# Performance work log

Hardware: AMD Instinct MI355X
Metric: run time of the kernel (lower is better)

The kernel has to match this reference:

```python
import jax, jax.numpy as jnp
import numpy as np

N, A, AD, D, H, KTOP = 5, 900, 8, 256, 8, 300


def _bbox_min_max(anchor):
    # anchor: [N,A,8] = x,y,z,logw,logl,logh,sin_yaw,cos_yaw
    xyz = anchor[..., :3]
    w, l, h = [jnp.exp(anchor[..., i]) for i in (3, 4, 5)]
    sy, cy = anchor[..., 6], anchor[..., 7]
    yaw = jnp.arctan2(sy, cy)
    ca, sa = jnp.abs(jnp.cos(yaw)), jnp.abs(jnp.sin(yaw))
    ex = 0.5 * (l * ca + w * sa)
    ey = 0.5 * (l * sa + w * ca)
    half = jnp.stack([ex, ey, 0.5 * h], axis=-1)
    return xyz - half, xyz + half


def _forward(i2j_anchor, b_anchor, b_feature, transform_matrix, anchor_embed,
             w_roi, b_roi, bn_g, bn_b, fc1_w, fc1_b, fc2_w, fc2_b,
             anc_w, anc_b, lam_w, lam_b, wq, bq, wk, bk, wv, bv, wo, bo,
             ln_g, ln_b, K):
    n, a, ad = b_anchor.shape
    d = b_feature.shape[-1]
    heads = lam_w.shape[-1]
    dh = d // heads
    # ROI scoring + topk selection of anchors to broadcast to neighbors
    roi = jax.nn.sigmoid(b_feature @ w_roi + b_roi)[..., 0]              # [N,A]
    top_scores, top_idx = jax.lax.top_k(roi, K)                          # [N,K]
    conf = top_scores > 0.5                                              # [N,K]
    nbr = jnp.take_along_axis(b_feature, top_idx[..., None], axis=1)     # [N,K,D]
    idx4 = jnp.broadcast_to(top_idx[None, :, :, None], (n, n, K, ad))
    i2j_sel = jnp.take_along_axis(i2j_anchor, idx4, axis=2)              # [N,N,K,AD]
    # remove self (eye-mask): off-diagonal j per row i, row-major order
    offdiag = np.array([[j for j in range(n) if j != i] for i in range(n)])
    rows = np.arange(n)[:, None]
    m = K * (n - 1)
    i2j_rm = i2j_sel[rows, offdiag].reshape(n, m, ad)                    # [N,M,AD]
    tm_rm = transform_matrix[rows, offdiag]                              # [N,N-1,4,4]
    key_feat = nbr[offdiag].reshape(n, m, d)                             # [N,M,D]
    conf_rm = conf[offdiag].reshape(n, m, 1)
    nf_masked = key_feat * conf_rm
    # bbox-range masked aggregation of neighbor features into ego anchors
    mn, mx = _bbox_min_max(b_anchor)                                     # [N,A,3]
    centers = i2j_rm[..., :3]                                            # [N,M,3]
    inside = jnp.all((centers[:, None, :, :] >= mn[:, :, None, :]) &
                     (centers[:, None, :, :] <= mx[:, :, None, :]), axis=-1)  # [N,A,M]
    agg = jnp.einsum('nam,nmd->nad', inside.astype(b_feature.dtype), nf_masked)
    is_greater_than_range = ~jnp.any(inside, axis=1)                     # [N,M]
    b_feature = b_feature + agg
    # transform-matrix encoding: first 3 rows of 4x4 -> BN -> MLP
    mlp_in = tm_rm[:, :, :3, :].reshape(-1, 12)
    mu = mlp_in.mean(0)
    var = mlp_in.var(0)
    xbn = (mlp_in - mu) / jnp.sqrt(var + 1e-5) * bn_g + bn_b
    t = jax.nn.relu(xbn @ fc1_w + fc1_b) @ fc2_w + fc2_b                 # [N*(N-1),D]
    trans_enc = jnp.repeat(t.reshape(n, n - 1, 1, d), K, axis=2).reshape(n, m, d)
    key_pos = i2j_rm @ anc_w + anc_b + trans_enc                         # anchorencoder + trans
    # distance-biased attention mask
    diff = b_anchor[:, :, None, :2] - i2j_rm[:, None, :, :2]
    dist = jnp.sqrt(jnp.sum(diff * diff, axis=-1) + 1e-12)               # cdist [N,A,M]
    lm = (b_feature @ lam_w + lam_b).transpose(0, 2, 1)                  # [N,H,A]
    bias = -jnp.log1p(dist)[:, None, :, :] * lm[..., None]               # [N,H,A,M]
    # multi-head attention (query=b_feature(+anchor_embed pos), key/value=neighbors)
    q = b_feature + anchor_embed
    k = key_feat + key_pos
    v = key_feat
    qh = (q @ wq + bq).reshape(n, a, heads, dh)
    kh = (k @ wk + bk).reshape(n, m, heads, dh)
    vh = (v @ wv + bv).reshape(n, m, heads, dh)
    logits = jnp.einsum('nahd,nmhd->nham', qh, kh) / np.sqrt(dh).astype(np.float32) + bias
    attn = jax.nn.softmax(logits, axis=-1)
    out = jnp.einsum('nham,nmhd->nahd', attn, vh).reshape(n, a, d) @ wo + bo
    res = b_feature + out                                                # residual (identity=query)
    mu2 = res.mean(-1, keepdims=True)
    var2 = res.var(-1, keepdims=True)
    return (res - mu2) / jnp.sqrt(var2 + 1e-5) * ln_g + ln_b


def setup_inputs() -> dict:
    key = jax.random.key(0)
    ks = jax.random.split(key, 24)
    s = 0.05
    inp = {
        'i2j_anchor': jax.random.normal(ks[0], (N, N, A, AD), jnp.float32),
        'b_anchor': jax.random.normal(ks[1], (N, A, AD), jnp.float32),
        'b_feature': jax.random.normal(ks[2], (N, A, D), jnp.float32),
        'transform_matrix': jax.random.normal(ks[3], (N, N, 4, 4), jnp.float32),
        'anchor_embed': jax.random.normal(ks[4], (N, A, D), jnp.float32),
        'w_roi': jax.random.normal(ks[5], (D, 1), jnp.float32) * s,
        'b_roi': jnp.zeros((1,), jnp.float32),
        'bn_g': jnp.ones((12,), jnp.float32),
        'bn_b': jnp.zeros((12,), jnp.float32),
        'fc1_w': jax.random.normal(ks[6], (12, D), jnp.float32) * s,
        'fc1_b': jnp.zeros((D,), jnp.float32),
        'fc2_w': jax.random.normal(ks[7], (D, D), jnp.float32) * s,
        'fc2_b': jnp.zeros((D,), jnp.float32),
        'anc_w': jax.random.normal(ks[8], (AD, D), jnp.float32) * s,
        'anc_b': jnp.zeros((D,), jnp.float32),
        'lam_w': jax.random.normal(ks[9], (D, H), jnp.float32) * s,
        'lam_b': jnp.zeros((H,), jnp.float32),
        'wq': jax.random.normal(ks[10], (D, D), jnp.float32) * s,
        'bq': jnp.zeros((D,), jnp.float32),
        'wk': jax.random.normal(ks[11], (D, D), jnp.float32) * s,
        'bk': jnp.zeros((D,), jnp.float32),
        'wv': jax.random.normal(ks[12], (D, D), jnp.float32) * s,
        'bv': jnp.zeros((D,), jnp.float32),
        'wo': jax.random.normal(ks[13], (D, D), jnp.float32) * s,
        'bo': jnp.zeros((D,), jnp.float32),
        'ln_g': jnp.ones((D,), jnp.float32),
        'ln_b': jnp.zeros((D,), jnp.float32),
        'K': KTOP,
    }
    return inp


def reference(i2j_anchor, b_anchor, b_feature, transform_matrix, anchor_embed,
              w_roi, b_roi, bn_g, bn_b, fc1_w, fc1_b, fc2_w, fc2_b,
              anc_w, anc_b, lam_w, lam_b, wq, bq, wk, bk, wv, bv, wo, bo,
              ln_g, ln_b, K):
    return _forward(i2j_anchor, b_anchor, b_feature, transform_matrix, anchor_embed,
                    w_roi, b_roi, bn_g, bn_b, fc1_w, fc1_b, fc2_w, fc2_b,
                    anc_w, anc_b, lam_w, lam_b, wq, bq, wk, bk, wv, bv, wo, bo,
                    ln_g, ln_b, K)
```

## Files before the change

### kernel.cpp

```cpp
#include <hip/hip_runtime.h>
#include <math.h>

#define N_ 5
#define A_ 900
#define AD_ 8
#define D_ 256
#define H_ 8
#define DH_ 32
#define K_ 300
#define NM1_ 4
#define M_ 1200
#define MP_ 1216
#define KC_ 64
#define HALF_ 600
#define NCHUNK2_ 10

typedef _Float16 f16x8 __attribute__((ext_vector_type(8)));
typedef _Float16 f16x4 __attribute__((ext_vector_type(4)));
typedef float f32x4 __attribute__((ext_vector_type(4)));

__global__ __launch_bounds__(256) void score_kernel(const float* __restrict__ bf,
                                                    const float* __restrict__ w,
                                                    const float* __restrict__ b,
                                                    float* __restrict__ scores) {
  int wid = threadIdx.x >> 6, lane = threadIdx.x & 63;
  int row = blockIdx.x * 4 + wid;
  if (row >= N_ * A_) return;
  const float* x = bf + (long)row * D_;
  float dot = 0.f;
#pragma unroll
  for (int t = 0; t < 4; t++) dot += x[lane + 64 * t] * w[lane + 64 * t];
#pragma unroll
  for (int o = 32; o; o >>= 1) dot += __shfl_xor(dot, o, 64);
  if (lane == 0) scores[row] = 1.0f / (1.0f + expf(-(dot + b[0])));
}

__global__ __launch_bounds__(1024) void topk_kernel(const float* __restrict__ scores,
                                                    int* __restrict__ top_idx,
                                                    float* __restrict__ conf) {
  __shared__ float sc[1024];
  __shared__ int si[1024];
  int i = blockIdx.x, t = threadIdx.x;
  sc[t] = (t < A_) ? scores[i * A_ + t] : -INFINITY;
  si[t] = t;
  __syncthreads();
  for (int k = 2; k <= 1024; k <<= 1) {
    for (int j = k >> 1; j > 0; j >>= 1) {
      int ixj = t ^ j;
      if (ixj > t) {
        bool dir = ((t & k) == 0);
        float a = sc[t], b = sc[ixj];
        bool sw = dir ? (a < b) : (a > b);
        if (sw) {
          sc[t] = b; sc[ixj] = a;
          int tmp = si[t]; si[t] = si[ixj]; si[ixj] = tmp;
        }
      }
      __syncthreads();
    }
  }
  if (t < K_) {
    top_idx[i * K_ + t] = si[t];
    conf[i * K_ + t] = sc[t] > 0.5f ? 1.0f : 0.0f;
  }
}

__global__ __launch_bounds__(256) void mlp_kernel(const float* __restrict__ tm,
                                                  const float* __restrict__ bn_g, const float* __restrict__ bn_b,
                                                  const float* __restrict__ fc1_w, const float* __restrict__ fc1_b,
                                                  const float* __restrict__ fc2_w, const float* __restrict__ fc2_b,
                                                  float* __restrict__ t_out) {
  int r = blockIdx.x;
  int t = threadIdx.x;
  __shared__ float x[20][12];
  __shared__ float y[12];
  __shared__ float hbuf[D_];
  if (t < 240) {
    int rr = t / 12, f = t % 12;
    int i = rr / NM1_, jj = rr % NM1_;
    int j = jj < i ? jj : jj + 1;
    int r4 = f / 4, c4 = f % 4;
    x[rr][f] = tm[((long)(i * N_ + j) * 4 + r4) * 4 + c4];
  }
  __syncthreads();
  if (t < 12) {
    float s = 0.f;
    for (int rr = 0; rr < 20; rr++) s += x[rr][t];
    float m = s / 20.0f;
    float v = 0.f;
    for (int rr = 0; rr < 20; rr++) { float d = x[rr][t] - m; v += d * d; }
    v /= 20.0f;
    y[t] = (x[r][t] - m) * rsqrtf(v + 1e-5f) * bn_g[t] + bn_b[t];
  }
  __syncthreads();
  float acc = fc1_b[t];
#pragma unroll
  for (int f = 0; f < 12; f++) acc += y[f] * fc1_w[f * D_ + t];
  hbuf[t] = fmaxf(acc, 0.0f);
  __syncthreads();
  float acc2 = fc2_b[t];
  for (int k = 0; k < D_; k++) acc2 += hbuf[k] * fc2_w[k * D_ + t];
  t_out[r * D_ + t] = acc2;
}

#define GKT_ 30
__global__ __launch_bounds__(256) void gather_kernel(const float* __restrict__ b_feature,
                                                     const float* __restrict__ i2j_anchor,
                                                     const int* __restrict__ top_idx,
                                                     const float* __restrict__ conf,
                                                     const float* __restrict__ anc_w,
                                                     const float* __restrict__ anc_b,
                                                     const float* __restrict__ t_mlp,
                                                     _Float16* __restrict__ key_feat16,
                                                     float* __restrict__ conf_rm,
                                                     float* __restrict__ i2j_rm,
                                                     _Float16* __restrict__ key_in16) {
  int blk = blockIdx.x;
  int i = blk / NM1_, jj = blk % NM1_;
  int j = jj < i ? jj : jj + 1;
  int k0 = blockIdx.y * GKT_;
  int c = threadIdx.x;
  __shared__ float aw[AD_][D_];
#pragma unroll
  for (int r = 0; r < AD_; r++) aw[r][c] = anc_w[r * D_ + c];
  float ab = anc_b[c];
  float tv = t_mlp[(i * NM1_ + jj) * D_ + c];
  __syncthreads();
  for (int k = k0; k < k0 + GKT_; k++) {
    int idx = top_idx[j * K_ + k];
    float cf = conf[j * K_ + k];
    const float* src = b_feature + ((long)(j * A_ + idx)) * D_;
    float val = src[c];
    long mrow = (long)i * M_ + jj * K_ + k;
    key_feat16[mrow * D_ + c] = (_Float16)val;
    const float* ap = i2j_anchor + ((long)((i * N_ + j) * A_ + idx)) * AD_;
    if (c < AD_) i2j_rm[mrow * AD_ + c] = ap[c];
    if (c == 0) conf_rm[mrow] = cf;
    float pos = ab + tv;
#pragma unroll
    for (int r = 0; r < AD_; r++) pos += ap[r] * aw[r][c];
    key_in16[mrow * D_ + c] = (_Float16)(val + pos);
  }
}

__global__ __launch_bounds__(256) void trans_kernel(const float* __restrict__ w0, const float* __restrict__ w1,
                                                    const float* __restrict__ w2, const float* __restrict__ w3,
                                                    const _Float16* __restrict__ kf,
                                                    _Float16* __restrict__ wT, _Float16* __restrict__ kT) {
  int bid = blockIdx.x;
  int t = threadIdx.x;
  if (bid < 64) {
    int y = bid >> 4, tile = bid & 15;
    const float* src = (y == 0) ? w0 : (y == 1) ? w1 : (y == 2) ? w2 : w3;
    _Float16* dst = wT + (size_t)y * D_ * D_;
    int kr = (tile >> 2) * 64, nc = (tile & 3) * 64;
    __shared__ float lds[64][65];
#pragma unroll
    for (int r = 0; r < 16; r++) {
      int row = r * 4 + (t >> 6), col = t & 63;
      lds[row][col] = src[(size_t)(kr + row) * D_ + nc + col];
    }
    __syncthreads();
#pragma unroll
    for (int r = 0; r < 16; r++) {
      int orow = r * 4 + (t >> 6), ocol = t & 63;
      dst[(size_t)(nc + orow) * D_ + kr + ocol] = (_Float16)lds[ocol][orow];
    }
  } else {
    int b = bid - 64;
    int i = b / 76, rem = b % 76;
    int m0 = (rem % 19) * 64, d0 = (rem / 19) * 64;
    __shared__ _Float16 lds2[64][66];
    const _Float16* src = kf + (size_t)i * M_ * D_;
    _Float16* dst = kT + (size_t)i * D_ * M_;
#pragma unroll
    for (int r = 0; r < 16; r++) {
      int row = r * 4 + (t >> 6), col = t & 63;
      int m = m0 + row;
      lds2[row][col] = (m < M_) ? src[(size_t)m * D_ + d0 + col] : (_Float16)0.0f;
    }
    __syncthreads();
#pragma unroll
    for (int r = 0; r < 16; r++) {
      int orow = r * 4 + (t >> 6), ocol = t & 63;
      int m = m0 + ocol;
      if (m < M_) dst[(size_t)(d0 + orow) * M_ + m] = lds2[ocol][orow];
    }
  }
}

__global__ __launch_bounds__(256) void insbias_kernel(const float* __restrict__ i2j_rm,
                                                      const float* __restrict__ conf_rm,
                                                      const float* __restrict__ ban,
                                                      _Float16* __restrict__ inside,
                                                      _Float16* __restrict__ Lbuf) {
  int i = blockIdx.x;
  int g = blockIdx.y;
  __shared__ float cx[M_], cy[M_], cz[M_], cf[M_];
  for (int m = threadIdx.x; m < M_; m += 256) {
    const float* cp = i2j_rm + ((long)i * M_ + m) * AD_;
    cx[m] = cp[0]; cy[m] = cp[1]; cz[m] = cp[2];
    cf[m] = conf_rm[(long)i * M_ + m];
  }
  __syncthreads();
#pragma unroll
  for (int r = 0; r < 4; r++) {
    int a = g * 4 + r;
    int row = i * A_ + a;
    const float* ap = ban + (long)row * AD_;
    float ax = ap[0], ay = ap[1], az = ap[2];
    float w = expf(ap[3]), l = expf(ap[4]), hh = expf(ap[5]);
    float yaw = atan2f(ap[6], ap[7]);
    float ca = fabsf(cosf(yaw)), sa = fabsf(sinf(yaw));
    float ex = 0.5f * (l * ca + w * sa);
    float ey = 0.5f * (l * sa + w * ca);
    float ez = 0.5f * hh;
    float mn0 = ax - ex, mn1 = ay - ey, mn2 = az - ez;
    float mx0 = ax + ex, mx1 = ay + ey, mx2 = az + ez;
    _Float16* ldst = Lbuf + (size_t)row * MP_;
    _Float16* idst = inside + (size_t)row * M_;
    for (int m = threadIdx.x; m < M_; m += 256) {
      float c0 = cx[m], c1 = cy[m], c2 = cz[m];
      bool ins = (c0 >= mn0) && (c0 <= mx0) && (c1 >= mn1) && (c1 <= mx1) && (c2 >= mn2) && (c2 <= mx2);
      idst[m] = ins ? (_Float16)cf[m] : (_Float16)0.0f;
      float dx = ax - c0, dy = ay - c1;
      ldst[m] = (_Float16)log1pf(sqrtf(dx * dx + dy * dy + 1e-12f));
    }
  }
}

#define GLD_ 74
template <typename TO, bool HAS_BIAS, bool HAS_RES>
__device__ __forceinline__ void gemm_tile_body(
    const _Float16* __restrict__ A, int lda, int Mr,
    const _Float16* __restrict__ B, int ldb,
    const float* __restrict__ bias, const float* __restrict__ res,
    TO* __restrict__ C, int ldc,
    int m0, int n0, int k_begin, int k_end) {
  __shared__ _Float16 As[64 * GLD_];
  __shared__ _Float16 Bs[64 * GLD_];
  int tid = threadIdx.x;
  int lane = tid & 63;
  int wid = tid >> 6;
  int wr = (wid >> 1) * 32, wc = (wid & 1) * 32;
  int lr = lane & 15, lk = (lane >> 4) * 8;
  int srow = tid >> 3;
  int scol = (tid & 7) * 8;
  f16x8 aR[2], bR[2];
  f16x8 zero8 = {};
  auto loadg = [&](int kb) {
#pragma unroll
    for (int r = 0; r < 2; r++) {
      int gm = m0 + srow + r * 32;
      int gk = kb + scol;
      aR[r] = (gm < Mr && gk < k_end) ? *(const f16x8*)&A[(size_t)gm * lda + gk] : zero8;
      int gn = n0 + srow + r * 32;
      bR[r] = (gk < k_end) ? *(const f16x8*)&B[(size_t)gn * ldb + gk] : zero8;
    }
  };
  auto store_lds = [&]() {
#pragma unroll
    for (int r = 0; r < 2; r++) {
      *(f16x8*)&As[(srow + r * 32) * GLD_ + scol] = aR[r];
      *(f16x8*)&Bs[(srow + r * 32) * GLD_ + scol] = bR[r];
    }
  };
  f32x4 acc[2][2] = {};
  int niter = (k_end - k_begin + 63) >> 6;
  loadg(k_begin);
  store_lds();
  __syncthreads();
  for (int it = 0; it < niter; ++it) {
    bool more = (it + 1 < niter);
    if (more) loadg(k_begin + (it + 1) * 64);
#pragma unroll
    for (int ks = 0; ks < 2; ks++) {
      f16x8 af[2], bf[2];
#pragma unroll
      for (int mi = 0; mi < 2; mi++) af[mi] = *(const f16x8*)&As[(wr + mi * 16 + lr) * GLD_ + ks * 32 + lk];
#pragma unroll
      for (int ni = 0; ni < 2; ni++) bf[ni] = *(const f16x8*)&Bs[(wc + ni * 16 + lr) * GLD_ + ks * 32 + lk];
#pragma unroll
      for (int mi = 0; mi < 2; mi++)
#pragma unroll
        for (int ni = 0; ni < 2; ni++)
          acc[mi][ni] = __builtin_amdgcn_mfma_f32_16x16x32_f16(af[mi], bf[ni], acc[mi][ni], 0, 0, 0);
    }
    __syncthreads();
    if (more) { store_lds(); __syncthreads(); }
  }
#pragma unroll
  for (int mi = 0; mi < 2; mi++)
#pragma unroll
    for (int ni = 0; ni < 2; ni++)
#pragma unroll
      for (int rr = 0; rr < 4; rr++) {
        int row = m0 + wr + mi * 16 + (lane >> 4) * 4 + rr;
        int col = n0 + wc + ni * 16 + lr;
        if (row < Mr) {
          float v = acc[mi][ni][rr];
          if (HAS_BIAS) v += bias[col];
          if (HAS_RES) v += res[(size_t)row * ldc + col];
          C[(size_t)row * ldc + col] = (TO)v;
        }
      }
}

__global__ __launch_bounds__(256) void agg_kernel(const _Float16* __restrict__ inside16,
                                                  const _Float16* __restrict__ kT16,
                                                  float* __restrict__ partial) {
  int i = blockIdx.z >> 2, sk = blockIdx.z & 3;
  int kb = sk * 320;
  int ke = kb + 320 < M_ ? kb + 320 : M_;
  gemm_tile_body<float, false, false>(
      inside16 + (size_t)i * A_ * M_, M_, A_,
      kT16 + (size_t)i * D_ * M_, M_,
      nullptr, nullptr,
      partial + (size_t)(sk * N_ + i) * A_ * D_, D_,
      blockIdx.x * 64, blockIdx.y * 64, kb, ke);
}

__global__ __launch_bounds__(256) void agg_reduce(const float* __restrict__ partial,
                                                  const float* __restrict__ b_feature,
                                                  const float* __restrict__ anchor_embed,
                                                  const float* __restrict__ lam_w,
                                                  const float* __restrict__ lam_b,
                                                  float* __restrict__ bf_upd,
                                                  _Float16* __restrict__ qin16,
                                                  float* __restrict__ lm_rm) {
  int wid = threadIdx.x >> 6, lane = threadIdx.x & 63;
  int rg = blockIdx.x * 4 + wid;
  int d0 = lane * 4;
  float lw[4][8];
#pragma unroll
  for (int e = 0; e < 4; e++) {
#pragma unroll
    for (int h = 0; h < 8; h++) lw[e][h] = lam_w[(d0 + e) * 8 + h];
  }
  float4 s = *(const float4*)&partial[(size_t)rg * D_ + d0];
#pragma unroll
  for (int sk = 1; sk < 4; sk++) {
    float4 p = *(const float4*)&partial[((size_t)sk * N_ * A_ + rg) * D_ + d0];
    s.x += p.x; s.y += p.y; s.z += p.z; s.w += p.w;
  }
  float4 bf = *(const float4*)&b_feature[(size_t)rg * D_ + d0];
  s.x += bf.x; s.y += bf.y; s.z += bf.z; s.w += bf.w;
  *(float4*)&bf_upd[(size_t)rg * D_ + d0] = s;
  float4 ae = *(const float4*)&anchor_embed[(size_t)rg * D_ + d0];
  f16x4 q4;
  q4[0] = (_Float16)(s.x + ae.x); q4[1] = (_Float16)(s.y + ae.y);
  q4[2] = (_Float16)(s.z + ae.z); q4[3] = (_Float16)(s.w + ae.w);
  *(f16x4*)&qin16[(size_t)rg * D_ + d0] = q4;
  float sv[4] = {s.x, s.y, s.z, s.w};
  float acc[8] = {};
#pragma unroll
  for (int e = 0; e < 4; e++)
#pragma unroll
    for (int h = 0; h < 8; h++) acc[h] += sv[e] * lw[e][h];
#pragma unroll
  for (int h = 0; h < 8; h++) {
#pragma unroll
    for (int o = 32; o; o >>= 1) acc[h] += __shfl_xor(acc[h], o, 64);
  }
  if (lane == 0) {
#pragma unroll
    for (int h = 0; h < 8; h++) lm_rm[(size_t)rg * H_ + h] = acc[h] + lam_b[h];
  }
}

__global__ __launch_bounds__(256) void qkv_kernel(const _Float16* __restrict__ qA,
                                                  const _Float16* __restrict__ kA,
                                                  const _Float16* __restrict__ vA,
                                                  const _Float16* __restrict__ wT,
                                                  const float* __restrict__ bq,
                                                  const float* __restrict__ bk,
                                                  const float* __restrict__ bv,
                                                  _Float16* __restrict__ qC,
                                                  _Float16* __restrict__ kC,
                                                  _Float16* __restrict__ vC) {
  int bid = blockIdx.x;
  const _Float16 *Ap, *Bp;
  const float* bias;
  _Float16* Cp;
  int Mr, t, mt, nt;
  if (bid < 284)      { Ap = qA; Bp = wT;               bias = bq; Cp = qC; Mr = 4500; t = bid;       mt = t % 71; nt = t / 71; }
  else if (bid < 660) { Ap = kA; Bp = wT + D_ * D_;     bias = bk; Cp = kC; Mr = 6000; t = bid - 284; mt = t % 94; nt = t / 94; }
  else                { Ap = vA; Bp = wT + 2 * D_ * D_; bias = bv; Cp = vC; Mr = 6000; t = bid - 660; mt = t % 94; nt = t / 94; }
  gemm_tile_body<_Float16, true, false>(Ap, D_, Mr, Bp, D_, bias, nullptr, Cp, D_, mt * 64, nt * 64, 0, D_);
}

__global__ __launch_bounds__(256) void outp_kernel(const _Float16* __restrict__ att16,
                                                   const _Float16* __restrict__ woT,
                                                   float* __restrict__ partial2) {
  int bid = blockIdx.x;
  int sk = bid >= 284 ? 1 : 0;
  int t = bid - sk * 284;
  int mt = t % 71, nt = t / 71;
  gemm_tile_body<float, false, false>(att16, D_, 4500, woT, D_, nullptr, nullptr,
                                      partial2 + (size_t)sk * 4500 * D_, D_,
                                      mt * 64, nt * 64, sk * 128, sk * 128 + 128);
}

__global__ __launch_bounds__(256) void attn_mfma(const _Float16* __restrict__ qh16,
                                                 const _Float16* __restrict__ kh16,
                                                 const _Float16* __restrict__ vh16,
                                                 const float* __restrict__ lm_rm,
                                                 const _Float16* __restrict__ Lbuf,
                                                 float* __restrict__ part_ms,
                                                 float* __restrict__ part_o) {
  int bid = blockIdx.x;
  int wgid = (bid & 7) * 150 + (bid >> 3);
  int ih = wgid / 30;
  int rest = wgid % 30;
  int half = rest / 15, qt = rest % 15;
  int i = ih >> 3, h = ih & 7;
  int a0 = qt * 64;
  int mbase = half * HALF_;
  int mlimit = mbase + HALF_;

  __shared__ _Float16 QP[64][74];
  __shared__ _Float16 Ks[64][42];
  __shared__ _Float16 Vt[32][74];
  __shared__ _Float16 Ls[64][74];
  __shared__ float lmvs[64];

  int tid = threadIdx.x;
  int lane = tid & 63;
  int w16 = (tid >> 6) * 16;
  int lr = lane & 15;
  int lk = (lane >> 4) * 8;
  int srow = tid >> 2, spiece = tid & 3;
  int lrow = tid >> 3, lpc = (tid & 7) * 8;

  {
    int aq = a0 + srow;
    int a_ld = aq < A_ ? aq : A_ - 1;
    const uint4* src = (const uint4*)(qh16 + ((long)(i * A_ + a_ld) * D_ + h * DH_));
    *(uint4*)&QP[srow][spiece * 8] = src[spiece];
  }
  if (tid < 64) {
    int aq = a0 + tid;
    int a_ld = aq < A_ ? aq : A_ - 1;
    lmvs[tid] = lm_rm[(long)(i * A_ + a_ld) * H_ + h];
  }

  const _Float16* kb = kh16 + (long)i * M_ * D_ + h * DH_;
  const _Float16* vb = vh16 + (long)i * M_ * D_ + h * DH_;
  const _Float16* lptr[2];
#pragma unroll
  for (int rr = 0; rr < 2; rr++) {
    int aq = a0 + lrow + rr * 32;
    int a_ld = aq < A_ ? aq : A_ - 1;
    lptr[rr] = Lbuf + (size_t)(i * A_ + a_ld) * MP_ + lpc;
  }

  uint4 kvR, vvR;
  f16x8 lR[2];
  auto loadr = [&](int c) {
    int m0 = mbase + c * KC_;
    int mrow = m0 + srow;
    if (mrow < M_) {
      kvR = ((const uint4*)(kb + (long)mrow * D_))[spiece];
      vvR = ((const uint4*)(vb + (long)mrow * D_))[spiece];
    } else {
      kvR = make_uint4(0, 0, 0, 0);
      vvR = make_uint4(0, 0, 0, 0);
    }
#pragma unroll
    for (int rr = 0; rr < 2; rr++) lR[rr] = *(const f16x8*)&lptr[rr][m0];
  };

  __syncthreads();

  float lmr[4];
#pragma unroll
  for (int r = 0; r < 4; r++) lmr[r] = lmvs[w16 + (lane >> 4) * 4 + r];
  f16x8 qa = *(const f16x8*)&QP[w16 + lr][lk];

  float m_run[4], s_part[4];
  f32x4 oacc[2] = {};
#pragma unroll
  for (int r = 0; r < 4; r++) { m_run[r] = -INFINITY; s_part[r] = 0.0f; }

  loadr(0);

  for (int c = 0; c < NCHUNK2_; c++) {
    int m0 = mbase + c * KC_;
    __syncthreads();
    *(uint4*)&Ks[srow][spiece * 8] = kvR;
    {
      const _Float16* hp = (const _Float16*)&vvR;
#pragma unroll
      for (int e = 0; e < 8; e++) Vt[spiece * 8 + e][srow] = hp[e];
    }
#pragma unroll
    for (int rr = 0; rr < 2; rr++) *(f16x8*)&Ls[lrow + rr * 32][lpc] = lR[rr];
    if (c + 1 < NCHUNK2_) loadr(c + 1);
    __syncthreads();

    f32x4 sacc[4];
#pragma unroll
    for (int mb = 0; mb < 4; mb++) {
      f16x8 kf = *(const f16x8*)&Ks[mb * 16 + lr][lk];
      sacc[mb] = __builtin_amdgcn_mfma_f32_16x16x32_f16(qa, kf, (f32x4){0.f, 0.f, 0.f, 0.f}, 0, 0, 0);
    }

    float lg[4][4];
#pragma unroll
    for (int mb = 0; mb < 4; mb++) {
      int mcol = m0 + mb * 16 + (lane & 15);
      bool valid = (mcol < mlimit);
#pragma unroll
      for (int r = 0; r < 4; r++) {
        int qrow = w16 + (lane >> 4) * 4 + r;
        float L = (float)Ls[qrow][mb * 16 + (lane & 15)];
        float v = sacc[mb][r] * 0.17677669529663687f - L * lmr[r];
        lg[mb][r] = valid ? v : -INFINITY;
      }
    }
#pragma unroll
    for (int r = 0; r < 4; r++) {
      float cm = fmaxf(fmaxf(lg[0][r], lg[1][r]), fmaxf(lg[2][r], lg[3][r]));
#pragma unroll
      for (int o = 1; o < 16; o <<= 1) cm = fmaxf(cm, __shfl_xor(cm, o, 64));
      float nm = fmaxf(m_run[r], cm);
      float corr = __expf(m_run[r] - nm);
      s_part[r] *= corr;
      oacc[0][r] *= corr;
      oacc[1][r] *= corr;
      m_run[r] = nm;
      float ps = 0.0f;
#pragma unroll
      for (int mb = 0; mb < 4; mb++) {
        float p = __expf(lg[mb][r] - nm);
        ps += p;
        QP[w16 + (lane >> 4) * 4 + r][mb * 16 + (lane & 15)] = (_Float16)p;
      }
      s_part[r] += ps;
    }

#pragma unroll
    for (int ks = 0; ks < 2; ks++) {
      f16x8 pa = *(const f16x8*)&QP[w16 + lr][ks * 32 + lk];
#pragma unroll
      for (int db = 0; db < 2; db++) {
        f16x8 vf = *(const f16x8*)&Vt[db * 16 + lr][ks * 32 + lk];
        oacc[db] = __builtin_amdgcn_mfma_f32_16x16x32_f16(pa, vf, oacc[db], 0, 0, 0);
      }
    }
  }

  size_t base = (size_t)(half * 40 + ih) * A_;
#pragma unroll
  for (int r = 0; r < 4; r++) {
    float st = s_part[r];
#pragma unroll
    for (int o = 1; o < 16; o <<= 1) st += __shfl_xor(st, o, 64);
    int a = a0 + w16 + (lane >> 4) * 4 + r;
    if (a < A_) {
      size_t rowb = base + a;
      if ((lane & 15) == 0) {
        part_ms[rowb * 2 + 0] = m_run[r];
        part_ms[rowb * 2 + 1] = st;
      }
      part_o[rowb * 32 + (lane & 15)] = oacc[0][r];
      part_o[rowb * 32 + 16 + (lane & 15)] = oacc[1][r];
    }
  }
}

__global__ __launch_bounds__(256) void attn_merge(const float* __restrict__ part_ms,
                                                  const float* __restrict__ part_o,
                                                  _Float16* __restrict__ att16) {
  int t = threadIdx.x;
  int R = blockIdx.x * 8 + (t >> 5);
  int d = t & 31;
  int ih = R / A_, a = R % A_;
  int i = ih >> 3, h = ih & 7;
  size_t r0 = (size_t)ih * A_ + a;
  size_t r1 = (size_t)(40 + ih) * A_ + a;
  float m0 = part_ms[r0 * 2], s0 = part_ms[r0 * 2 + 1];
  float m1 = part_ms[r1 * 2], s1 = part_ms[r1 * 2 + 1];
  float M = fmaxf(m0, m1);
  float e0 = __expf(m0 - M), e1 = __expf(m1 - M);
  float inv = 1.0f / (s0 * e0 + s1 * e1);
  float o = part_o[r0 * 32 + d] * e0 + part_o[r1 * 32 + d] * e1;
  att16[((size_t)(i * A_ + a)) * D_ + h * DH_ + d] = (_Float16)(o * inv);
}

__global__ __launch_bounds__(256) void ln_kernel(const float* __restrict__ partial2,
                                                 const float* __restrict__ bo,
                                                 const float* __restrict__ resid,
                                                 const float* __restrict__ g,
                                                 const float* __restrict__ b,
                                                 float* __restrict__ out) {
  int row = blockIdx.x;
  int t = threadIdx.x;
  size_t idx = (size_t)row * D_ + t;
  float v = partial2[idx] + partial2[(size_t)4500 * D_ + idx] + bo[t] + resid[idx];
  float s = v, sq = v * v;
#pragma unroll
  for (int o = 32; o; o >>= 1) {
    s += __shfl_xor(s, o, 64);
    sq += __shfl_xor(sq, o, 64);
  }
  __shared__ float ss[4], ssq[4];
  int wid = t >> 6, lane = t & 63;
  if (lane == 0) { ss[wid] = s; ssq[wid] = sq; }
  __syncthreads();
  float ts = ss[0] + ss[1] + ss[2] + ss[3];
  float tq = ssq[0] + ssq[1] + ssq[2] + ssq[3];
  float mean = ts / (float)D_;
  float var = tq / (float)D_ - mean * mean;
  out[idx] = (v - mean) * rsqrtf(var + 1e-5f) * g[t] + b[t];
}

extern "C" void kernel_launch(void* const* d_in, const int* in_sizes, int n_in,
                              void* d_out, int out_size, void* d_ws, size_t ws_size,
                              hipStream_t stream) {
  const float* i2j_anchor   = (const float*)d_in[0];
  const float* b_anchor     = (const float*)d_in[1];
  const float* b_feature    = (const float*)d_in[2];
  const float* tm           = (const float*)d_in[3];
  const float* anchor_embed = (const float*)d_in[4];
  const float* w_roi  = (const float*)d_in[5];
  const float* b_roi  = (const float*)d_in[6];
  const float* bn_g   = (const float*)d_in[7];
  const float* bn_b   = (const float*)d_in[8];
  const float* fc1_w  = (const float*)d_in[9];
  const float* fc1_b  = (const float*)d_in[10];
  const float* fc2_w  = (const float*)d_in[11];
  const float* fc2_b  = (const float*)d_in[12];
  const float* anc_w  = (const float*)d_in[13];
  const float* anc_b  = (const float*)d_in[14];
  const float* lam_w  = (const float*)d_in[15];
  const float* lam_b  = (const float*)d_in[16];
  const float* wq = (const float*)d_in[17];
  const float* bq = (const float*)d_in[18];
  const float* wk = (const float*)d_in[19];
  const float* bk = (const float*)d_in[20];
  const float* wv = (const float*)d_in[21];
  const float* bv = (const float*)d_in[22];
  const float* wo = (const float*)d_in[23];
  const float* bo = (const float*)d_in[24];
  const float* ln_g = (const float*)d_in[25];
  const float* ln_b = (const float*)d_in[26];

  float* ws = (float*)d_ws;
  size_t off = 0;
  auto alloc = [&](size_t n) { float* p = ws + off; off += (n + 3) & ~(size_t)3; return p; };

  float* scores     = alloc(N_ * A_);
  int*   top_idx    = (int*)alloc(N_ * K_);
  float* conf       = alloc(N_ * K_);
  float* t_mlp      = alloc(20 * D_);
  float* conf_rm    = alloc((size_t)N_ * M_);
  float* i2j_rm     = alloc((size_t)N_ * M_ * AD_);
  _Float16* key_feat16 = (_Float16*)alloc((size_t)N_ * M_ * D_ / 2);
  _Float16* key_in16   = (_Float16*)alloc((size_t)N_ * M_ * D_ / 2);
  _Float16* kT16       = (_Float16*)alloc((size_t)N_ * D_ * M_ / 2);
  _Float16* inside16   = (_Float16*)alloc((size_t)N_ * A_ * M_ / 2);
  _Float16* wT16       = (_Float16*)alloc((size_t)4 * D_ * D_ / 2);
  _Float16* Lbuf16     = (_Float16*)alloc((size_t)N_ * A_ * MP_ / 2 + 16);
  float* partial    = alloc((size_t)4 * N_ * A_ * D_);
  float* bf_upd     = alloc((size_t)N_ * A_ * D_);
  _Float16* qin16   = (_Float16*)alloc((size_t)N_ * A_ * D_ / 2);
  _Float16* qh16    = (_Float16*)alloc((size_t)N_ * A_ * D_ / 2);
  _Float16* kh16    = (_Float16*)alloc((size_t)N_ * M_ * D_ / 2);
  _Float16* vh16    = (_Float16*)alloc((size_t)N_ * M_ * D_ / 2);
  float* lm_rm      = alloc((size_t)N_ * A_ * H_);
  _Float16* att16   = (_Float16*)alloc((size_t)N_ * A_ * D_ / 2);
  float* partial2   = alloc((size_t)2 * N_ * A_ * D_);
  float* part_ms    = alloc((size_t)2 * 40 * A_ * 2);
  float* part_o     = alloc((size_t)2 * 40 * A_ * 32);

  score_kernel<<<(N_ * A_ + 3) / 4, 256, 0, stream>>>(b_feature, w_roi, b_roi, scores);
  topk_kernel<<<N_, 1024, 0, stream>>>(scores, top_idx, conf);
  mlp_kernel<<<20, 256, 0, stream>>>(tm, bn_g, bn_b, fc1_w, fc1_b, fc2_w, fc2_b, t_mlp);
  gather_kernel<<<dim3(N_ * NM1_, K_ / GKT_), 256, 0, stream>>>(b_feature, i2j_anchor, top_idx, conf,
                                                                anc_w, anc_b, t_mlp,
                                                                key_feat16, conf_rm, i2j_rm, key_in16);
  trans_kernel<<<64 + 380, 256, 0, stream>>>(wq, wk, wv, wo, key_feat16, wT16, kT16);
  insbias_kernel<<<dim3(N_, A_ / 4), 256, 0, stream>>>(i2j_rm, conf_rm, b_anchor, inside16, Lbuf16);
  agg_kernel<<<dim3(15, 4, N_ * 4), 256, 0, stream>>>(inside16, kT16, partial);
  agg_reduce<<<(N_ * A_) / 4, 256, 0, stream>>>(partial, b_feature, anchor_embed, lam_w, lam_b,
                                                bf_upd, qin16, lm_rm);
  qkv_kernel<<<284 + 376 + 376, 256, 0, stream>>>(qin16, key_in16, key_feat16, wT16,
                                                  bq, bk, bv, qh16, kh16, vh16);
  attn_mfma<<<1200, 256, 0, stream>>>(qh16, kh16, vh16, lm_rm, Lbuf16, part_ms, part_o);
  attn_merge<<<(40 * A_) / 8, 256, 0, stream>>>(part_ms, part_o, att16);
  outp_kernel<<<568, 256, 0, stream>>>(att16, wT16 + 3 * D_ * D_, partial2);
  ln_kernel<<<N_ * A_, 256, 0, stream>>>(partial2, bo, bf_upd, ln_g, ln_b, (float*)d_out);
}
```

Measured before the change: 211.4 us.

## Transpose QK MFMA output so each lane owns one query row in softmax

Swaps the MFMA operands in the attention kernel so the score tile is transposed: each lane now holds four key columns of a single query row. Online softmax then needs only two cross-lane shuffles for the max and sum, and keeps one running max and sum per lane instead of four. L values and probabilities are read and written as 4-wide vectors. The correction factor is redistributed to the output accumulators via shuffles. LDS row strides change to 72/40, and the gather kernel's k-tile shrinks to 10 so more blocks are launched.

```diff
diff --git a/kernel.cpp b/kernel.cpp
--- a/kernel.cpp
+++ b/kernel.cpp
@@ -103,7 +103,7 @@
   t_out[r * D_ + t] = acc2;
 }
 
-#define GKT_ 30
+#define GKT_ 10
 __global__ __launch_bounds__(256) void gather_kernel(const float* __restrict__ b_feature,
                                                      const float* __restrict__ i2j_anchor,
                                                      const int* __restrict__ top_idx,
@@ -401,6 +401,8 @@
                                       mt * 64, nt * 64, sk * 128, sk * 128 + 128);
 }
 
+#define LQP_ 72
+#define LKS_ 40
 __global__ __launch_bounds__(256) void attn_mfma(const _Float16* __restrict__ qh16,
                                                  const _Float16* __restrict__ kh16,
                                                  const _Float16* __restrict__ vh16,
@@ -418,10 +420,10 @@
   int mbase = half * HALF_;
   int mlimit = mbase + HALF_;
 
-  __shared__ _Float16 QP[64][74];
-  __shared__ _Float16 Ks[64][42];
+  __shared__ _Float16 QP[64 * LQP_];
+  __shared__ _Float16 Ks[64 * LKS_];
   __shared__ _Float16 Vt[32][74];
-  __shared__ _Float16 Ls[64][74];
+  __shared__ _Float16 Ls[64 * LQP_];
   __shared__ float lmvs[64];
 
   int tid = threadIdx.x;
@@ -429,6 +431,7 @@
   int w16 = (tid >> 6) * 16;
   int lr = lane & 15;
   int lk = (lane >> 4) * 8;
+  int mq = (lane >> 4) * 4;
   int srow = tid >> 2, spiece = tid & 3;
   int lrow = tid >> 3, lpc = (tid & 7) * 8;
 
@@ -436,7 +439,7 @@
     int aq = a0 + srow;
     int a_ld = aq < A_ ? aq : A_ - 1;
     const uint4* src = (const uint4*)(qh16 + ((long)(i * A_ + a_ld) * D_ + h * DH_));
-    *(uint4*)&QP[srow][spiece * 8] = src[spiece];
+    *(uint4*)&QP[srow * LQP_ + spiece * 8] = src[spiece];
   }
   if (tid < 64) {
     int aq = a0 + tid;
@@ -472,76 +475,80 @@
 
   __syncthreads();
 
-  float lmr[4];
-#pragma unroll
-  for (int r = 0; r < 4; r++) lmr[r] = lmvs[w16 + (lane >> 4) * 4 + r];
-  f16x8 qa = *(const f16x8*)&QP[w16 + lr][lk];
-
-  float m_run[4], s_part[4];
+  int qrow = w16 + lr;
+  float lmv = lmvs[qrow];
+  f16x8 qa = *(const f16x8*)&QP[qrow * LQP_ + lk];
+
+  float m_run = -INFINITY, s_part = 0.0f;
   f32x4 oacc[2] = {};
-#pragma unroll
-  for (int r = 0; r < 4; r++) { m_run[r] = -INFINITY; s_part[r] = 0.0f; }
 
   loadr(0);
 
   for (int c = 0; c < NCHUNK2_; c++) {
     int m0 = mbase + c * KC_;
     __syncthreads();
-    *(uint4*)&Ks[srow][spiece * 8] = kvR;
+    *(uint4*)&Ks[srow * LKS_ + spiece * 8] = kvR;
     {
       const _Float16* hp = (const _Float16*)&vvR;
 #pragma unroll
       for (int e = 0; e < 8; e++) Vt[spiece * 8 + e][srow] = hp[e];
     }
 #pragma unroll
-    for (int rr = 0; rr < 2; rr++) *(f16x8*)&Ls[lrow + rr * 32][lpc] = lR[rr];
+    for (int rr = 0; rr < 2; rr++) *(f16x8*)&Ls[(lrow + rr * 32) * LQP_ + lpc] = lR[rr];
     if (c + 1 < NCHUNK2_) loadr(c + 1);
     __syncthreads();
 
     f32x4 sacc[4];
 #pragma unroll
     for (int mb = 0; mb < 4; mb++) {
-      f16x8 kf = *(const f16x8*)&Ks[mb * 16 + lr][lk];
-      sacc[mb] = __builtin_amdgcn_mfma_f32_16x16x32_f16(qa, kf, (f32x4){0.f, 0.f, 0.f, 0.f}, 0, 0, 0);
+      f16x8 kf = *(const f16x8*)&Ks[(mb * 16 + lr) * LKS_ + lk];
+      sacc[mb] = __builtin_amdgcn_mfma_f32_16x16x32_f16(kf, qa, (f32x4){0.f, 0.f, 0.f, 0.f}, 0, 0, 0);
     }
 
     float lg[4][4];
 #pragma unroll
     for (int mb = 0; mb < 4; mb++) {
-      int mcol = m0 + mb * 16 + (lane & 15);
-      bool valid = (mcol < mlimit);
-#pragma unroll
-      for (int r = 0; r < 4; r++) {
-        int qrow = w16 + (lane >> 4) * 4 + r;
-        float L = (float)Ls[qrow][mb * 16 + (lane & 15)];
-        float v = sacc[mb][r] * 0.17677669529663687f - L * lmr[r];
-        lg[mb][r] = valid ? v : -INFINITY;
+      f16x4 l4 = *(const f16x4*)&Ls[qrow * LQP_ + mb * 16 + mq];
+#pragma unroll
+      for (int rr = 0; rr < 4; rr++) {
+        int mcol = m0 + mb * 16 + mq + rr;
+        float v = sacc[mb][rr] * 0.17677669529663687f - (float)l4[rr] * lmv;
+        lg[mb][rr] = (mcol < mlimit) ? v : -INFINITY;
       }
     }
+    float cm = -INFINITY;
+#pragma unroll
+    for (int mb = 0; mb < 4; mb++)
+#pragma unroll
+      for (int rr = 0; rr < 4; rr++) cm = fmaxf(cm, lg[mb][rr]);
+    cm = fmaxf(cm, __shfl_xor(cm, 16, 64));
+    cm = fmaxf(cm, __shfl_xor(cm, 32, 64));
+    float nm = fmaxf(m_run, cm);
+    float corr = __expf(m_run - nm);
+    m_run = nm;
+    float ps = 0.0f;
+#pragma unroll
+    for (int mb = 0; mb < 4; mb++) {
+      f16x4 p4;
+#pragma unroll
+      for (int rr = 0; rr < 4; rr++) {
+        float p = __expf(lg[mb][rr] - nm);
+        ps += p;
+        p4[rr] = (_Float16)p;
+      }
+      *(f16x4*)&QP[qrow * LQP_ + mb * 16 + mq] = p4;
+    }
+    s_part = s_part * corr + ps;
 #pragma unroll
     for (int r = 0; r < 4; r++) {
-      float cm = fmaxf(fmaxf(lg[0][r], lg[1][r]), fmaxf(lg[2][r], lg[3][r]));
-#pragma unroll
-      for (int o = 1; o < 16; o <<= 1) cm = fmaxf(cm, __shfl_xor(cm, o, 64));
-      float nm = fmaxf(m_run[r], cm);
-      float corr = __expf(m_run[r] - nm);
-      s_part[r] *= corr;
-      oacc[0][r] *= corr;
-      oacc[1][r] *= corr;
-      m_run[r] = nm;
-      float ps = 0.0f;
-#pragma unroll
-      for (int mb = 0; mb < 4; mb++) {
-        float p = __expf(lg[mb][r] - nm);
-        ps += p;
-        QP[w16 + (lane >> 4) * 4 + r][mb * 16 + (lane & 15)] = (_Float16)p;
-      }
-      s_part[r] += ps;
+      float cr = __shfl(corr, (lane & 48) + mq + r, 64);
+      oacc[0][r] *= cr;
+      oacc[1][r] *= cr;
     }
 
 #pragma unroll
     for (int ks = 0; ks < 2; ks++) {
-      f16x8 pa = *(const f16x8*)&QP[w16 + lr][ks * 32 + lk];
+      f16x8 pa = *(const f16x8*)&QP[(w16 + lr) * LQP_ + ks * 32 + lk];
 #pragma unroll
       for (int db = 0; db < 2; db++) {
         f16x8 vf = *(const f16x8*)&Vt[db * 16 + lr][ks * 32 + lk];
@@ -550,21 +557,25 @@
     }
   }
 
+  float st = s_part;
+  st += __shfl_xor(st, 16, 64);
+  st += __shfl_xor(st, 32, 64);
+
   size_t base = (size_t)(half * 40 + ih) * A_;
+  if (lane < 16) {
+    int a = a0 + w16 + lane;
+    if (a < A_) {
+      part_ms[(base + a) * 2 + 0] = m_run;
+      part_ms[(base + a) * 2 + 1] = st;
+    }
+  }
 #pragma unroll
   for (int r = 0; r < 4; r++) {
-    float st = s_part[r];
-#pragma unroll
-    for (int o = 1; o < 16; o <<= 1) st += __shfl_xor(st, o, 64);
-    int a = a0 + w16 + (lane >> 4) * 4 + r;
+    int a = a0 + w16 + mq + r;
     if (a < A_) {
       size_t rowb = base + a;
-      if ((lane & 15) == 0) {
-        part_ms[rowb * 2 + 0] = m_run[r];
-        part_ms[rowb * 2 + 1] = st;
-      }
-      part_o[rowb * 32 + (lane & 15)] = oacc[0][r];
-      part_o[rowb * 32 + 16 + (lane & 15)] = oacc[1][r];
+      part_o[rowb * 32 + lr] = oacc[0][r];
+      part_o[rowb * 32 + 16 + lr] = oacc[1][r];
     }
   }
 }
```

Result: faster. 179.3 us (-15.2%).
